# Performance work log

Measured on AMD Instinct MI355X. Metric: run time of the kernel, lower is better.

The kernel has to match this reference:

```python
import jax, jax.numpy as jnp
from jax import lax
import numpy as np

EPSILON = 0.1
GAMMA = 1.0
RHO = 0.5
STOPERR = 1e-6
NUM_ITER_MAX = 1000


def setup_inputs() -> dict:
    key = jax.random.key(0)
    n, k = 131072, 512
    logits = jax.random.normal(key, (n, k), dtype=jnp.float32)
    return {"logits": logits}


def reference(logits):
    # logits is detached in the original (no grad through it)
    logits = lax.stop_gradient(logits)
    # cost = -log softmax over classes
    cost = -jax.nn.log_softmax(logits, axis=1)          # [n, k]
    n, k = cost.shape
    dt = cost.dtype

    # augment with a zero-cost dummy column (the "mu" column)
    expand_cost = jnp.concatenate([cost, jnp.zeros((n, 1), dt)], axis=1)  # [n, k+1]
    Q = jnp.exp(-expand_cost / EPSILON)                  # [n, k+1]

    Pa = jnp.full((n, 1), 1.0 / n, dt)                   # row marginal (equality)
    Pb = jnp.full((k + 1, 1), RHO / k, dt).at[-1].set(1.0 - RHO)  # col marginal
    b0 = jnp.full((k + 1, 1), 1.0 / (k + 1), dt)
    a0 = jnp.zeros((n, 1), dt)
    fi = GAMMA / (GAMMA + EPSILON)

    def cond(state):
        a, b, last_b, err, it = state
        return jnp.logical_and(err > STOPERR, it < NUM_ITER_MAX)

    def body(state):
        a, b, last_b, err, it = state
        a = Pa / (Q @ b)                                 # [n, 1]
        b = Pb / (Q.T @ a)                               # [k+1, 1]
        # semi-relaxed KL step on all but the dummy column
        b = b.at[:-1, :].set(jnp.power(b[:-1, :], fi))
        err = jnp.linalg.norm(b - last_b)
        return (a, b, b, err, it + 1)

    init = (a0, b0, b0, jnp.asarray(1.0, dt), jnp.asarray(0, jnp.int32))
    a, b, _, err, iternum = lax.while_loop(cond, body, init)

    plan = a * Q * b.T                                   # [n, k+1]
    plan = plan * n                                      # final=True scaling
    plan = plan[:, :-1].astype(jnp.float32)              # drop dummy column
    return plan
```

## Files before the change

### kernel.cpp

```cpp
#include <hip/hip_runtime.h>
#include <hip/hip_cooperative_groups.h>

constexpr int   NROWS   = 131072;
constexpr int   KCOLS   = 512;
constexpr int   KP1     = 513;
constexpr float PA      = 1.0f / 131072.0f;
constexpr float PB_REAL = 0.5f / 512.0f;
constexpr float PB_DUM  = 0.5f;
constexpr float FI      = (float)(1.0 / 1.1);
constexpr float STOPERR = 1e-6f;
constexpr int   MAXIT   = 1000;
constexpr float LOG2E   = 1.4426950408889634f;
constexpr float CQ      = 10.0f * LOG2E;
constexpr float LN2     = 0.6931471805599453f;

constexpr int BLOCKS  = 256;
constexpr int THREADS = 1024;
constexpr int WPB     = THREADS / 64;
constexpr int NWAVES  = BLOCKS * WPB;

constexpr size_t OFF_LSE = 0;
constexpr size_t OFF_A   = (size_t)NROWS;
constexpr int    KPAD    = 520;
constexpr size_t OFF_B0  = 2 * (size_t)NROWS;
constexpr size_t OFF_B1  = OFF_B0 + KPAD;
constexpr size_t OFF_BF  = OFF_B0 + 2 * KPAD;
constexpr size_t OFF_EP  = OFF_B0 + 3 * KPAD;
constexpr size_t OFF_CP  = OFF_B0 + 4 * KPAD;
constexpr size_t OFF_BAR = OFF_CP + (size_t)KP1 * BLOCKS;

constexpr size_t QLO_BYTE_OFF = (size_t)NROWS * KCOLS * 2;

__device__ __forceinline__ float waveReduceSum(float v) {
#pragma unroll
  for (int s = 32; s >= 1; s >>= 1) v += __shfl_xor(v, s);
  return v;
}
__device__ __forceinline__ float waveReduceMax(float v) {
#pragma unroll
  for (int s = 32; s >= 1; s >>= 1) v = fmaxf(v, __shfl_xor(v, s));
  return v;
}

__device__ __forceinline__ float scload(const float* p) {
  return __hip_atomic_load(p, __ATOMIC_RELAXED, __HIP_MEMORY_SCOPE_AGENT);
}
__device__ __forceinline__ void scstore(float* p, float v) {
  __hip_atomic_store(p, v, __ATOMIC_RELAXED, __HIP_MEMORY_SCOPE_AGENT);
}

__device__ __forceinline__ void unpack8(const uint4 h, const uint2 l, float q[8]) {
  q[0] = __uint_as_float((h.x << 16)         | ((l.x << 8) & 0xff00u));
  q[1] = __uint_as_float((h.x & 0xffff0000u) | ( l.x       & 0xff00u));
  q[2] = __uint_as_float((h.y << 16)         | ((l.x >> 8) & 0xff00u));
  q[3] = __uint_as_float((h.y & 0xffff0000u) | ((l.x >> 16)& 0xff00u));
  q[4] = __uint_as_float((h.z << 16)         | ((l.y << 8) & 0xff00u));
  q[5] = __uint_as_float((h.z & 0xffff0000u) | ( l.y       & 0xff00u));
  q[6] = __uint_as_float((h.w << 16)         | ((l.y >> 8) & 0xff00u));
  q[7] = __uint_as_float((h.w & 0xffff0000u) | ((l.y >> 16)& 0xff00u));
}

__global__ __launch_bounds__(1024) void lse_q_init_kernel(
    const float* __restrict__ logits, float* __restrict__ ws,
    unsigned short* __restrict__ qhi, unsigned char* __restrict__ qlo) {
  float* lse = ws + OFF_LSE;
  const int nw   = (gridDim.x * blockDim.x) >> 6;
  const int gw   = (blockIdx.x * blockDim.x + threadIdx.x) >> 6;
  const int lane = threadIdx.x & 63;

  for (int r = gw; r < NROWS; r += nw) {
    const float4* row4 = reinterpret_cast<const float4*>(logits + (size_t)r * KCOLS);
    float4 x0 = row4[lane];
    float4 x1 = row4[64 + lane];
    float m = fmaxf(fmaxf(fmaxf(x0.x, x0.y), fmaxf(x0.z, x0.w)),
                    fmaxf(fmaxf(x1.x, x1.y), fmaxf(x1.z, x1.w)));
    m = waveReduceMax(m);
    float s = exp2f((x0.x - m) * LOG2E) + exp2f((x0.y - m) * LOG2E)
            + exp2f((x0.z - m) * LOG2E) + exp2f((x0.w - m) * LOG2E)
            + exp2f((x1.x - m) * LOG2E) + exp2f((x1.y - m) * LOG2E)
            + exp2f((x1.z - m) * LOG2E) + exp2f((x1.w - m) * LOG2E);
    s = waveReduceSum(s);
    float L = m + log2f(s) * LN2;
    if (lane == 0) lse[r] = L;
    unsigned u[8];
    u[0] = __float_as_uint(exp2f((x0.x - L) * CQ)) + 0x80u;
    u[1] = __float_as_uint(exp2f((x0.y - L) * CQ)) + 0x80u;
    u[2] = __float_as_uint(exp2f((x0.z - L) * CQ)) + 0x80u;
    u[3] = __float_as_uint(exp2f((x0.w - L) * CQ)) + 0x80u;
    u[4] = __float_as_uint(exp2f((x1.x - L) * CQ)) + 0x80u;
    u[5] = __float_as_uint(exp2f((x1.y - L) * CQ)) + 0x80u;
    u[6] = __float_as_uint(exp2f((x1.z - L) * CQ)) + 0x80u;
    u[7] = __float_as_uint(exp2f((x1.w - L) * CQ)) + 0x80u;
    ushort4 hA, hB;  uchar4 lA, lB;
    hA.x = (unsigned short)(u[0] >> 16); lA.x = (unsigned char)(u[0] >> 8);
    hA.y = (unsigned short)(u[1] >> 16); lA.y = (unsigned char)(u[1] >> 8);
    hA.z = (unsigned short)(u[2] >> 16); lA.z = (unsigned char)(u[2] >> 8);
    hA.w = (unsigned short)(u[3] >> 16); lA.w = (unsigned char)(u[3] >> 8);
    hB.x = (unsigned short)(u[4] >> 16); lB.x = (unsigned char)(u[4] >> 8);
    hB.y = (unsigned short)(u[5] >> 16); lB.y = (unsigned char)(u[5] >> 8);
    hB.z = (unsigned short)(u[6] >> 16); lB.z = (unsigned char)(u[6] >> 8);
    hB.w = (unsigned short)(u[7] >> 16); lB.w = (unsigned char)(u[7] >> 8);
    *reinterpret_cast<ushort4*>(qhi + (size_t)r * KCOLS + 4 * lane)       = hA;
    *reinterpret_cast<ushort4*>(qhi + (size_t)r * KCOLS + 256 + 4 * lane) = hB;
    *reinterpret_cast<uchar4*>(qlo + (size_t)r * KCOLS + 4 * lane)        = lA;
    *reinterpret_cast<uchar4*>(qlo + (size_t)r * KCOLS + 256 + 4 * lane)  = lB;
  }
  if (blockIdx.x == 0 && threadIdx.x < KP1)
    ws[OFF_B0 + threadIdx.x] = 1.0f / 513.0f;
  if (blockIdx.x == 0 && threadIdx.x == 0) {
    ((unsigned*)(ws + OFF_BAR))[0] = 0u;
    ((unsigned*)(ws + OFF_BAR + 32))[0] = 0u;
  }
}

__global__ __launch_bounds__(THREADS, 4) void sinkhorn_loop(
    const unsigned short* __restrict__ qhi, const unsigned char* __restrict__ qlo,
    float* __restrict__ ws) {
  float* a    = ws + OFF_A;
  float* b0   = ws + OFF_B0;
  float* b1   = ws + OFF_B1;
  float* bfin = ws + OFF_BF;
  float* ep   = ws + OFF_EP;
  float* colp = ws + OFF_CP;
  unsigned* cnt = (unsigned*)(ws + OFF_BAR);
  unsigned* gen = (unsigned*)(ws + OFF_BAR + 32);

  __shared__ float lds[WPB][KPAD];
  __shared__ float s_err;
  __shared__ int   s_nbar;
  __shared__ int   s_dead;

  const int tid  = threadIdx.x;
  const int wv   = tid >> 6;
  const int lane = tid & 63;
  const int bk   = blockIdx.x;
  const int gw   = bk * WPB + wv;

  if (tid == 0) { s_nbar = 0; s_dead = 0; }
  __syncthreads();

  auto gridBar = [&]() {
    __syncthreads();
    if (tid == 0) {
      int nb = s_nbar;
      unsigned old = atomicAdd(cnt, 1u);
      if (old == (unsigned)(nb * BLOCKS + (BLOCKS - 1))) {
        atomicAdd(gen, 1u);
      } else if (!s_dead) {
        int spins = 0;
        while (__hip_atomic_load(gen, __ATOMIC_RELAXED, __HIP_MEMORY_SCOPE_AGENT)
               <= (unsigned)nb) {
          __builtin_amdgcn_s_sleep(1);
          if (++spins > (1 << 24)) { s_dead = 1; break; }
        }
      }
      s_nbar = nb + 1;
    }
    __syncthreads();
  };

  float err = 1.0f;
  int it = 0;
  for (; it < MAXIT; ++it) {
    if (!(err > STOPERR)) break;

    const float* bcv = (it & 1) ? b1 : b0;
    float*       bnv = (it & 1) ? b0 : b1;

    float rb[8];
#pragma unroll
    for (int e = 0; e < 8; ++e) rb[e] = scload(&bcv[8 * lane + e]);
    float bdum = scload(&bcv[512]);

    float cp[8] = {0.f, 0.f, 0.f, 0.f, 0.f, 0.f, 0.f, 0.f};
    float adum = 0.f;
    for (int r = gw; r < NROWS; r += 4 * NWAVES) {
      const int r1 = r + NWAVES, r2 = r + 2 * NWAVES, r3 = r + 3 * NWAVES;
      uint4 h0 = ((const uint4*)(qhi + (size_t)r  * KCOLS))[lane];
      uint4 h1 = ((const uint4*)(qhi + (size_t)r1 * KCOLS))[lane];
      uint4 h2 = ((const uint4*)(qhi + (size_t)r2 * KCOLS))[lane];
      uint4 h3 = ((const uint4*)(qhi + (size_t)r3 * KCOLS))[lane];
      uint2 l0 = ((const uint2*)(qlo + (size_t)r  * KCOLS))[lane];
      uint2 l1 = ((const uint2*)(qlo + (size_t)r1 * KCOLS))[lane];
      uint2 l2 = ((const uint2*)(qlo + (size_t)r2 * KCOLS))[lane];
      uint2 l3 = ((const uint2*)(qlo + (size_t)r3 * KCOLS))[lane];
      float q0[8], q1[8], q2[8], q3[8];
      unpack8(h0, l0, q0);
      unpack8(h1, l1, q1);
      unpack8(h2, l2, q2);
      unpack8(h3, l3, q3);
      float d0 = 0.f, d1 = 0.f, d2 = 0.f, d3 = 0.f;
#pragma unroll
      for (int e = 0; e < 8; ++e) {
        d0 = fmaf(q0[e], rb[e], d0);
        d1 = fmaf(q1[e], rb[e], d1);
        d2 = fmaf(q2[e], rb[e], d2);
        d3 = fmaf(q3[e], rb[e], d3);
      }
#pragma unroll
      for (int s = 32; s >= 1; s >>= 1) {
        d0 += __shfl_xor(d0, s);
        d1 += __shfl_xor(d1, s);
        d2 += __shfl_xor(d2, s);
        d3 += __shfl_xor(d3, s);
      }
      float ai0 = PA / (d0 + bdum);
      float ai1 = PA / (d1 + bdum);
      float ai2 = PA / (d2 + bdum);
      float ai3 = PA / (d3 + bdum);
      if (lane == 0) { a[r] = ai0; a[r1] = ai1; a[r2] = ai2; a[r3] = ai3; }
#pragma unroll
      for (int e = 0; e < 8; ++e) {
        cp[e] = fmaf(ai0, q0[e], cp[e]);
        cp[e] = fmaf(ai1, q1[e], cp[e]);
        cp[e] = fmaf(ai2, q2[e], cp[e]);
        cp[e] = fmaf(ai3, q3[e], cp[e]);
      }
      adum += (ai0 + ai1) + (ai2 + ai3);
    }
#pragma unroll
    for (int e = 0; e < 8; ++e) lds[wv][8 * lane + e] = cp[e];
    if (lane == 0) lds[wv][512] = adum;
    __syncthreads();
    for (int t = tid; t < KP1; t += THREADS) {
      float s = 0.f;
#pragma unroll
      for (int w2 = 0; w2 < WPB; ++w2) s += lds[w2][t];
      scstore(&colp[(size_t)t * BLOCKS + bk], s);
    }
    gridBar();

    {
      int jcol = (wv == 0) ? 2 * bk
               : (wv == 1) ? 2 * bk + 1
               : (bk == 0 && wv == 2) ? 512 : -1;
      if (jcol >= 0) {
        float s = 0.f;
#pragma unroll
        for (int e = 0; e < 4; ++e)
          s += scload(&colp[(size_t)jcol * BLOCKS + 4 * lane + e]);
        s = waveReduceSum(s);
        if (lane == 0) {
          float bj = (jcol < KCOLS) ? powf(PB_REAL / s, FI) : (PB_DUM / s);
          scstore(&bnv[jcol], bj);
          float d = bj - scload(&bcv[jcol]);
          scstore(&ep[jcol], d * d);
        }
      }
    }
    gridBar();

    if (wv == 0) {
      float s = 0.f;
      for (int t = lane; t < KP1; t += 64) s += scload(&ep[t]);
      s = waveReduceSum(s);
      if (lane == 0) s_err = sqrtf(s);
    }
    __syncthreads();
    err = s_err;
  }

  if (bk == 0) {
    const float* bf = (it & 1) ? b1 : b0;
    for (int t = tid; t < KP1; t += THREADS) bfin[t] = scload(&bf[t]);
  }
}

__global__ __launch_bounds__(1024) void plan_epilogue(
    const float* __restrict__ logits, const float* __restrict__ ws,
    float* __restrict__ out) {
  const float* lse  = ws + OFF_LSE;
  const float* a    = ws + OFF_A;
  const float* bfin = ws + OFF_BF;
  const int nw   = (gridDim.x * blockDim.x) >> 6;
  const int gw   = (blockIdx.x * blockDim.x + threadIdx.x) >> 6;
  const int lane = threadIdx.x & 63;

  const float4* b4 = reinterpret_cast<const float4*>(bfin);
  float4 rb0 = b4[lane];
  float4 rb1 = b4[64 + lane];

  for (int r = gw; r < NROWS; r += nw) {
    const float4* row4 = reinterpret_cast<const float4*>(logits + (size_t)r * KCOLS);
    float4*       out4 = reinterpret_cast<float4*>(out + (size_t)r * KCOLS);
    float L  = lse[r];
    float na = a[r] * (float)NROWS;
    float4 x0 = row4[lane];
    float4 x1 = row4[64 + lane];
    float4 o0, o1;
    o0.x = na * exp2f((x0.x - L) * CQ) * rb0.x;
    o0.y = na * exp2f((x0.y - L) * CQ) * rb0.y;
    o0.z = na * exp2f((x0.z - L) * CQ) * rb0.z;
    o0.w = na * exp2f((x0.w - L) * CQ) * rb0.w;
    o1.x = na * exp2f((x1.x - L) * CQ) * rb1.x;
    o1.y = na * exp2f((x1.y - L) * CQ) * rb1.y;
    o1.z = na * exp2f((x1.z - L) * CQ) * rb1.z;
    o1.w = na * exp2f((x1.w - L) * CQ) * rb1.w;
    out4[lane]      = o0;
    out4[64 + lane] = o1;
  }
}

extern "C" void kernel_launch(void* const* d_in, const int* in_sizes, int n_in,
                              void* d_out, int out_size, void* d_ws, size_t ws_size,
                              hipStream_t stream) {
  (void)in_sizes; (void)n_in; (void)out_size; (void)ws_size;
  const float*    logits = (const float*)d_in[0];
  float*          out    = (float*)d_out;
  float*          ws     = (float*)d_ws;
  unsigned short* qhi    = (unsigned short*)d_out;
  unsigned char*  qlo    = (unsigned char*)d_out + QLO_BYTE_OFF;

  hipLaunchKernelGGL(lse_q_init_kernel, dim3(1024), dim3(1024), 0, stream,
                     logits, ws, qhi, qlo);

  const unsigned short* qhArg = qhi;
  const unsigned char*  qlArg = qlo;
  float*                wsArg = ws;
  void* args[] = { (void*)&qhArg, (void*)&qlArg, (void*)&wsArg };
  hipLaunchCooperativeKernel((void*)sinkhorn_loop, dim3(BLOCKS), dim3(THREADS),
                             args, 0, stream);

  hipLaunchKernelGGL(plan_epilogue, dim3(2048), dim3(1024), 0, stream,
                     logits, ws, out);
}
```

Baseline: 18.17 ms.

## Add geometric extrapolation of Sinkhorn b updates and unroll row loop to 8

```diff
diff --git a/kernel.cpp b/kernel.cpp
--- a/kernel.cpp
+++ b/kernel.cpp
@@ -25,11 +25,12 @@
 constexpr size_t OFF_B0  = 2 * (size_t)NROWS;
 constexpr size_t OFF_B1  = OFF_B0 + KPAD;
 constexpr size_t OFF_BF  = OFF_B0 + 2 * KPAD;
-constexpr size_t OFF_EP  = OFF_B0 + 3 * KPAD;
-constexpr size_t OFF_CP  = OFF_B0 + 4 * KPAD;
-constexpr size_t OFF_BAR = OFF_CP + (size_t)KP1 * BLOCKS;
-
-constexpr size_t QLO_BYTE_OFF = (size_t)NROWS * KCOLS * 2;
+constexpr size_t OFF_D0  = OFF_B0 + 3 * KPAD;
+constexpr size_t OFF_D1  = OFF_B0 + 4 * KPAD;
+
+constexpr size_t QLO_BYTE_OFF  = (size_t)NROWS * KCOLS * 2;
+constexpr size_t COLP_BYTE_OFF = 192ull * 1024 * 1024;
+constexpr size_t BAR_BYTE_OFF  = 200ull * 1024 * 1024;
 
 __device__ __forceinline__ float waveReduceSum(float v) {
 #pragma unroll
@@ -62,7 +63,8 @@
 
 __global__ __launch_bounds__(1024) void lse_q_init_kernel(
     const float* __restrict__ logits, float* __restrict__ ws,
-    unsigned short* __restrict__ qhi, unsigned char* __restrict__ qlo) {
+    unsigned short* __restrict__ qhi, unsigned char* __restrict__ qlo,
+    unsigned* __restrict__ bar) {
   float* lse = ws + OFF_LSE;
   const int nw   = (gridDim.x * blockDim.x) >> 6;
   const int gw   = (blockIdx.x * blockDim.x + threadIdx.x) >> 6;
@@ -108,25 +110,25 @@
   if (blockIdx.x == 0 && threadIdx.x < KP1)
     ws[OFF_B0 + threadIdx.x] = 1.0f / 513.0f;
   if (blockIdx.x == 0 && threadIdx.x == 0) {
-    ((unsigned*)(ws + OFF_BAR))[0] = 0u;
-    ((unsigned*)(ws + OFF_BAR + 32))[0] = 0u;
+    bar[0]  = 0u;
+    bar[32] = 0u;
   }
 }
 
 __global__ __launch_bounds__(THREADS, 4) void sinkhorn_loop(
     const unsigned short* __restrict__ qhi, const unsigned char* __restrict__ qlo,
-    float* __restrict__ ws) {
+    float* __restrict__ ws, float* __restrict__ colp, unsigned* __restrict__ bar) {
   float* a    = ws + OFF_A;
   float* b0   = ws + OFF_B0;
   float* b1   = ws + OFF_B1;
   float* bfin = ws + OFF_BF;
-  float* ep   = ws + OFF_EP;
-  float* colp = ws + OFF_CP;
-  unsigned* cnt = (unsigned*)(ws + OFF_BAR);
-  unsigned* gen = (unsigned*)(ws + OFF_BAR + 32);
+  float* dl0  = ws + OFF_D0;
+  float* dl1  = ws + OFF_D1;
+  unsigned* cnt = bar;
+  unsigned* gen = bar + 32;
 
   __shared__ float lds[WPB][KPAD];
-  __shared__ float s_err;
+  __shared__ float s_err, s_s1, s_s2;
   __shared__ int   s_nbar;
   __shared__ int   s_dead;
 
@@ -166,6 +168,8 @@
 
     const float* bcv = (it & 1) ? b1 : b0;
     float*       bnv = (it & 1) ? b0 : b1;
+    float*       dcu = (it & 1) ? dl1 : dl0;
+    const float* dpr = (it & 1) ? dl0 : dl1;
 
     float rb[8];
 #pragma unroll
@@ -174,49 +178,44 @@
 
     float cp[8] = {0.f, 0.f, 0.f, 0.f, 0.f, 0.f, 0.f, 0.f};
     float adum = 0.f;
-    for (int r = gw; r < NROWS; r += 4 * NWAVES) {
-      const int r1 = r + NWAVES, r2 = r + 2 * NWAVES, r3 = r + 3 * NWAVES;
-      uint4 h0 = ((const uint4*)(qhi + (size_t)r  * KCOLS))[lane];
-      uint4 h1 = ((const uint4*)(qhi + (size_t)r1 * KCOLS))[lane];
-      uint4 h2 = ((const uint4*)(qhi + (size_t)r2 * KCOLS))[lane];
-      uint4 h3 = ((const uint4*)(qhi + (size_t)r3 * KCOLS))[lane];
-      uint2 l0 = ((const uint2*)(qlo + (size_t)r  * KCOLS))[lane];
-      uint2 l1 = ((const uint2*)(qlo + (size_t)r1 * KCOLS))[lane];
-      uint2 l2 = ((const uint2*)(qlo + (size_t)r2 * KCOLS))[lane];
-      uint2 l3 = ((const uint2*)(qlo + (size_t)r3 * KCOLS))[lane];
-      float q0[8], q1[8], q2[8], q3[8];
-      unpack8(h0, l0, q0);
-      unpack8(h1, l1, q1);
-      unpack8(h2, l2, q2);
-      unpack8(h3, l3, q3);
-      float d0 = 0.f, d1 = 0.f, d2 = 0.f, d3 = 0.f;
-#pragma unroll
-      for (int e = 0; e < 8; ++e) {
-        d0 = fmaf(q0[e], rb[e], d0);
-        d1 = fmaf(q1[e], rb[e], d1);
-        d2 = fmaf(q2[e], rb[e], d2);
-        d3 = fmaf(q3[e], rb[e], d3);
+    for (int r = gw; r < NROWS; r += 8 * NWAVES) {
+      uint4 h[8];  uint2 l[8];
+#pragma unroll
+      for (int u = 0; u < 8; ++u) {
+        const int rr = r + u * NWAVES;
+        h[u] = ((const uint4*)(qhi + (size_t)rr * KCOLS))[lane];
+        l[u] = ((const uint2*)(qlo + (size_t)rr * KCOLS))[lane];
+      }
+      float d[8];
+#pragma unroll
+      for (int u = 0; u < 8; ++u) {
+        float q[8];
+        unpack8(h[u], l[u], q);
+        float dd = 0.f;
+#pragma unroll
+        for (int e = 0; e < 8; ++e) dd = fmaf(q[e], rb[e], dd);
+        d[u] = dd;
       }
 #pragma unroll
       for (int s = 32; s >= 1; s >>= 1) {
-        d0 += __shfl_xor(d0, s);
-        d1 += __shfl_xor(d1, s);
-        d2 += __shfl_xor(d2, s);
-        d3 += __shfl_xor(d3, s);
-      }
-      float ai0 = PA / (d0 + bdum);
-      float ai1 = PA / (d1 + bdum);
-      float ai2 = PA / (d2 + bdum);
-      float ai3 = PA / (d3 + bdum);
-      if (lane == 0) { a[r] = ai0; a[r1] = ai1; a[r2] = ai2; a[r3] = ai3; }
-#pragma unroll
-      for (int e = 0; e < 8; ++e) {
-        cp[e] = fmaf(ai0, q0[e], cp[e]);
-        cp[e] = fmaf(ai1, q1[e], cp[e]);
-        cp[e] = fmaf(ai2, q2[e], cp[e]);
-        cp[e] = fmaf(ai3, q3[e], cp[e]);
-      }
-      adum += (ai0 + ai1) + (ai2 + ai3);
+#pragma unroll
+        for (int u = 0; u < 8; ++u) d[u] += __shfl_xor(d[u], s);
+      }
+      float ai[8];
+#pragma unroll
+      for (int u = 0; u < 8; ++u) ai[u] = PA / (d[u] + bdum);
+      if (lane == 0) {
+#pragma unroll
+        for (int u = 0; u < 8; ++u) a[r + u * NWAVES] = ai[u];
+      }
+#pragma unroll
+      for (int u = 0; u < 8; ++u) {
+        float q[8];
+        unpack8(h[u], l[u], q);
+#pragma unroll
+        for (int e = 0; e < 8; ++e) cp[e] = fmaf(ai[u], q[e], cp[e]);
+        adum += ai[u];
+      }
     }
 #pragma unroll
     for (int e = 0; e < 8; ++e) lds[wv][8 * lane + e] = cp[e];
@@ -243,21 +242,44 @@
         if (lane == 0) {
           float bj = (jcol < KCOLS) ? powf(PB_REAL / s, FI) : (PB_DUM / s);
           scstore(&bnv[jcol], bj);
-          float d = bj - scload(&bcv[jcol]);
-          scstore(&ep[jcol], d * d);
+          scstore(&dcu[jcol], bj - scload(&bcv[jcol]));
         }
       }
     }
     gridBar();
 
     if (wv == 0) {
-      float s = 0.f;
-      for (int t = lane; t < KP1; t += 64) s += scload(&ep[t]);
-      s = waveReduceSum(s);
-      if (lane == 0) s_err = sqrtf(s);
+      float s0 = 0.f, s1 = 0.f, s2 = 0.f;
+      for (int t = lane; t < KP1; t += 64) {
+        float dc = scload(&dcu[t]);
+        float dp = scload(&dpr[t]);
+        s0 += dc * dc;  s1 += dc * dp;  s2 += dp * dp;
+      }
+#pragma unroll
+      for (int s = 32; s >= 1; s >>= 1) {
+        s0 += __shfl_xor(s0, s);
+        s1 += __shfl_xor(s1, s);
+        s2 += __shfl_xor(s2, s);
+      }
+      if (lane == 0) { s_err = sqrtf(s0); s_s1 = s1; s_s2 = s2; }
     }
     __syncthreads();
     err = s_err;
+
+    if ((it & 7) == 7 && err > 10.0f * STOPERR) {
+      float rho = (s_s2 > 0.f) ? (s_s1 / s_s2) : 0.f;
+      if (rho > 0.5f && rho < 0.95f) {
+        float c = rho / (1.0f - rho);
+        int jcol = (wv == 0) ? 2 * bk
+                 : (wv == 1) ? 2 * bk + 1
+                 : (bk == 0 && wv == 2) ? 512 : -1;
+        if (jcol >= 0 && lane == 0) {
+          float bx = scload(&bnv[jcol]) + c * scload(&dcu[jcol]);
+          if (bx > 1e-30f) scstore(&bnv[jcol], bx);
+        }
+        gridBar();
+      }
+    }
   }
 
   if (bk == 0) {
@@ -310,14 +332,19 @@
   float*          ws     = (float*)d_ws;
   unsigned short* qhi    = (unsigned short*)d_out;
   unsigned char*  qlo    = (unsigned char*)d_out + QLO_BYTE_OFF;
+  float*          colp   = (float*)((char*)d_out + COLP_BYTE_OFF);
+  unsigned*       bar    = (unsigned*)((char*)d_out + BAR_BYTE_OFF);
 
   hipLaunchKernelGGL(lse_q_init_kernel, dim3(1024), dim3(1024), 0, stream,
-                     logits, ws, qhi, qlo);
+                     logits, ws, qhi, qlo, bar);
 
   const unsigned short* qhArg = qhi;
   const unsigned char*  qlArg = qlo;
   float*                wsArg = ws;
-  void* args[] = { (void*)&qhArg, (void*)&qlArg, (void*)&wsArg };
+  float*                cpArg = colp;
+  unsigned*             brArg = bar;
+  void* args[] = { (void*)&qhArg, (void*)&qlArg, (void*)&wsArg,
+                   (void*)&cpArg, (void*)&brArg };
   hipLaunchCooperativeKernel((void*)sinkhorn_loop, dim3(BLOCKS), dim3(THREADS),
                              args, 0, stream);
 
```

After: 22.81 ms. 25.5% more time.

## Add Aitken-style b extrapolation and scale Sinkhorn loop to 512 blocks

Applied to the files above, without the earlier changes.

```diff
diff --git a/kernel.cpp b/kernel.cpp
--- a/kernel.cpp
+++ b/kernel.cpp
@@ -14,22 +14,21 @@
 constexpr float CQ      = 10.0f * LOG2E;
 constexpr float LN2     = 0.6931471805599453f;
 
-constexpr int BLOCKS  = 256;
 constexpr int THREADS = 1024;
 constexpr int WPB     = THREADS / 64;
-constexpr int NWAVES  = BLOCKS * WPB;
 
 constexpr size_t OFF_LSE = 0;
 constexpr size_t OFF_A   = (size_t)NROWS;
-constexpr int    KPAD    = 520;
+constexpr int    KPAD    = 516;
 constexpr size_t OFF_B0  = 2 * (size_t)NROWS;
 constexpr size_t OFF_B1  = OFF_B0 + KPAD;
 constexpr size_t OFF_BF  = OFF_B0 + 2 * KPAD;
-constexpr size_t OFF_EP  = OFF_B0 + 3 * KPAD;
-constexpr size_t OFF_CP  = OFF_B0 + 4 * KPAD;
-constexpr size_t OFF_BAR = OFF_CP + (size_t)KP1 * BLOCKS;
-
-constexpr size_t QLO_BYTE_OFF = (size_t)NROWS * KCOLS * 2;
+constexpr size_t OFF_D0  = OFF_B0 + 3 * KPAD;
+constexpr size_t OFF_D1  = OFF_B0 + 4 * KPAD;
+
+constexpr size_t QLO_BYTE_OFF  = (size_t)NROWS * KCOLS * 2;
+constexpr size_t COLP_BYTE_OFF = 192ull * 1024 * 1024;
+constexpr size_t BAR_BYTE_OFF  = 200ull * 1024 * 1024;
 
 __device__ __forceinline__ float waveReduceSum(float v) {
 #pragma unroll
@@ -62,7 +61,8 @@
 
 __global__ __launch_bounds__(1024) void lse_q_init_kernel(
     const float* __restrict__ logits, float* __restrict__ ws,
-    unsigned short* __restrict__ qhi, unsigned char* __restrict__ qlo) {
+    unsigned short* __restrict__ qhi, unsigned char* __restrict__ qlo,
+    unsigned* __restrict__ bar) {
   float* lse = ws + OFF_LSE;
   const int nw   = (gridDim.x * blockDim.x) >> 6;
   const int gw   = (blockIdx.x * blockDim.x + threadIdx.x) >> 6;
@@ -108,24 +108,25 @@
   if (blockIdx.x == 0 && threadIdx.x < KP1)
     ws[OFF_B0 + threadIdx.x] = 1.0f / 513.0f;
   if (blockIdx.x == 0 && threadIdx.x == 0) {
-    ((unsigned*)(ws + OFF_BAR))[0] = 0u;
-    ((unsigned*)(ws + OFF_BAR + 32))[0] = 0u;
-  }
-}
-
-__global__ __launch_bounds__(THREADS, 4) void sinkhorn_loop(
+    bar[0]  = 0u;
+    bar[32] = 0u;
+  }
+}
+
+template <int NBLK>
+__global__ __launch_bounds__(THREADS, 8) void sinkhorn_loop(
     const unsigned short* __restrict__ qhi, const unsigned char* __restrict__ qlo,
-    float* __restrict__ ws) {
+    float* __restrict__ ws, float* __restrict__ colp, unsigned* __restrict__ bar) {
   float* a    = ws + OFF_A;
   float* b0   = ws + OFF_B0;
   float* b1   = ws + OFF_B1;
   float* bfin = ws + OFF_BF;
-  float* ep   = ws + OFF_EP;
-  float* colp = ws + OFF_CP;
-  unsigned* cnt = (unsigned*)(ws + OFF_BAR);
-  unsigned* gen = (unsigned*)(ws + OFF_BAR + 32);
-
-  __shared__ float lds[WPB][KPAD];
+  float* dl0  = ws + OFF_D0;
+  float* dl1  = ws + OFF_D1;
+  unsigned* cnt = bar;
+  unsigned* gen = bar + 32;
+
+  __shared__ float lds[8][KPAD];
   __shared__ float s_err;
   __shared__ int   s_nbar;
   __shared__ int   s_dead;
@@ -135,6 +136,7 @@
   const int lane = tid & 63;
   const int bk   = blockIdx.x;
   const int gw   = bk * WPB + wv;
+  const int NWV  = NBLK * WPB;
 
   if (tid == 0) { s_nbar = 0; s_dead = 0; }
   __syncthreads();
@@ -144,7 +146,7 @@
     if (tid == 0) {
       int nb = s_nbar;
       unsigned old = atomicAdd(cnt, 1u);
-      if (old == (unsigned)(nb * BLOCKS + (BLOCKS - 1))) {
+      if (old == (unsigned)(nb * NBLK + (NBLK - 1))) {
         atomicAdd(gen, 1u);
       } else if (!s_dead) {
         int spins = 0;
@@ -166,6 +168,8 @@
 
     const float* bcv = (it & 1) ? b1 : b0;
     float*       bnv = (it & 1) ? b0 : b1;
+    float*       dcu = (it & 1) ? dl1 : dl0;
+    const float* dpr = (it & 1) ? dl0 : dl1;
 
     float rb[8];
 #pragma unroll
@@ -174,8 +178,8 @@
 
     float cp[8] = {0.f, 0.f, 0.f, 0.f, 0.f, 0.f, 0.f, 0.f};
     float adum = 0.f;
-    for (int r = gw; r < NROWS; r += 4 * NWAVES) {
-      const int r1 = r + NWAVES, r2 = r + 2 * NWAVES, r3 = r + 3 * NWAVES;
+    for (int r = gw; r < NROWS; r += 4 * NWV) {
+      const int r1 = r + NWV, r2 = r + 2 * NWV, r3 = r + 3 * NWV;
       uint4 h0 = ((const uint4*)(qhi + (size_t)r  * KCOLS))[lane];
       uint4 h1 = ((const uint4*)(qhi + (size_t)r1 * KCOLS))[lane];
       uint4 h2 = ((const uint4*)(qhi + (size_t)r2 * KCOLS))[lane];
@@ -218,46 +222,76 @@
       }
       adum += (ai0 + ai1) + (ai2 + ai3);
     }
-#pragma unroll
-    for (int e = 0; e < 8; ++e) lds[wv][8 * lane + e] = cp[e];
-    if (lane == 0) lds[wv][512] = adum;
+    if (wv >= 8) {
+#pragma unroll
+      for (int e = 0; e < 8; ++e) lds[wv - 8][8 * lane + e] = cp[e];
+      if (lane == 0) lds[wv - 8][512] = adum;
+    }
+    __syncthreads();
+    if (wv < 8) {
+#pragma unroll
+      for (int e = 0; e < 8; ++e) cp[e] += lds[wv][8 * lane + e];
+      if (lane == 0) adum += lds[wv][512];
+    }
+    __syncthreads();
+    if (wv < 8) {
+#pragma unroll
+      for (int e = 0; e < 8; ++e) lds[wv][8 * lane + e] = cp[e];
+      if (lane == 0) lds[wv][512] = adum;
+    }
     __syncthreads();
     for (int t = tid; t < KP1; t += THREADS) {
       float s = 0.f;
 #pragma unroll
-      for (int w2 = 0; w2 < WPB; ++w2) s += lds[w2][t];
-      scstore(&colp[(size_t)t * BLOCKS + bk], s);
+      for (int w2 = 0; w2 < 8; ++w2) s += lds[w2][t];
+      scstore(&colp[(size_t)t * NBLK + bk], s);
     }
     gridBar();
 
     {
-      int jcol = (wv == 0) ? 2 * bk
-               : (wv == 1) ? 2 * bk + 1
-               : (bk == 0 && wv == 2) ? 512 : -1;
-      if (jcol >= 0) {
+      const int jcol = bk + wv * NBLK;
+      if (jcol < KP1) {
         float s = 0.f;
 #pragma unroll
-        for (int e = 0; e < 4; ++e)
-          s += scload(&colp[(size_t)jcol * BLOCKS + 4 * lane + e]);
+        for (int e = 0; e < NBLK / 64; ++e)
+          s += scload(&colp[(size_t)jcol * NBLK + 64 * e + lane]);
         s = waveReduceSum(s);
         if (lane == 0) {
           float bj = (jcol < KCOLS) ? powf(PB_REAL / s, FI) : (PB_DUM / s);
           scstore(&bnv[jcol], bj);
-          float d = bj - scload(&bcv[jcol]);
-          scstore(&ep[jcol], d * d);
+          scstore(&dcu[jcol], bj - scload(&bcv[jcol]));
         }
       }
     }
     gridBar();
 
     if (wv == 0) {
-      float s = 0.f;
-      for (int t = lane; t < KP1; t += 64) s += scload(&ep[t]);
-      s = waveReduceSum(s);
-      if (lane == 0) s_err = sqrtf(s);
+      float s0 = 0.f;
+      for (int t = lane; t < KP1; t += 64) {
+        float dc = scload(&dcu[t]);
+        s0 += dc * dc;
+      }
+      s0 = waveReduceSum(s0);
+      if (lane == 0) s_err = sqrtf(s0);
     }
     __syncthreads();
     err = s_err;
+
+    if ((it & 7) == 7 && it >= 15 && err > 100.0f * STOPERR) {
+      const int jcol = bk + wv * NBLK;
+      if (jcol < KP1 && lane == 0) {
+        float dc = scload(&dcu[jcol]);
+        float dp = scload(&dpr[jcol]);
+        if (fabsf(dp) > 1e-37f) {
+          float rr = dc / dp;
+          if (rr > -0.97f && rr < 0.95f) {
+            float bx = scload(&bnv[jcol]) + (rr / (1.0f - rr)) * dc;
+            if (bx > 1e-30f) scstore(&bnv[jcol], bx);
+          }
+        }
+      }
+      gridBar();
+    }
   }
 
   if (bk == 0) {
@@ -310,16 +344,34 @@
   float*          ws     = (float*)d_ws;
   unsigned short* qhi    = (unsigned short*)d_out;
   unsigned char*  qlo    = (unsigned char*)d_out + QLO_BYTE_OFF;
+  float*          colp   = (float*)((char*)d_out + COLP_BYTE_OFF);
+  unsigned*       bar    = (unsigned*)((char*)d_out + BAR_BYTE_OFF);
 
   hipLaunchKernelGGL(lse_q_init_kernel, dim3(1024), dim3(1024), 0, stream,
-                     logits, ws, qhi, qlo);
+                     logits, ws, qhi, qlo, bar);
 
   const unsigned short* qhArg = qhi;
   const unsigned char*  qlArg = qlo;
   float*                wsArg = ws;
-  void* args[] = { (void*)&qhArg, (void*)&qlArg, (void*)&wsArg };
-  hipLaunchCooperativeKernel((void*)sinkhorn_loop, dim3(BLOCKS), dim3(THREADS),
-                             args, 0, stream);
+  float*                cpArg = colp;
+  unsigned*             brArg = bar;
+  void* args[] = { (void*)&qhArg, (void*)&qlArg, (void*)&wsArg,
+                   (void*)&cpArg, (void*)&brArg };
+
+  void (*k512)(const unsigned short*, const unsigned char*, float*, float*,
+               unsigned*) = sinkhorn_loop<512>;
+  void (*k256)(const unsigned short*, const unsigned char*, float*, float*,
+               unsigned*) = sinkhorn_loop<256>;
+  int nbPerCU = 0;
+  (void)hipOccupancyMaxActiveBlocksPerMultiprocessor(&nbPerCU, (const void*)k512,
+                                                     THREADS, 0);
+  if (nbPerCU >= 2) {
+    hipLaunchCooperativeKernel((void*)k512, dim3(512), dim3(THREADS),
+                               args, 0, stream);
+  } else {
+    hipLaunchCooperativeKernel((void*)k256, dim3(256), dim3(THREADS),
+                               args, 0, stream);
+  }
 
   hipLaunchKernelGGL(plan_epilogue, dim3(2048), dim3(1024), 0, stream,
                      logits, ws, out);
```

Measured after the change: 38.58 ms. +112.3%, slower.

## Pack Q as contiguous 24-bit rows per wave and stream via async global-to-LDS ring

Applied to the files above, without the earlier changes.

```diff
diff --git a/kernel.cpp b/kernel.cpp
--- a/kernel.cpp
+++ b/kernel.cpp
@@ -1,5 +1,4 @@
 #include <hip/hip_runtime.h>
-#include <hip/hip_cooperative_groups.h>
 
 constexpr int   NROWS   = 131072;
 constexpr int   KCOLS   = 512;
@@ -16,8 +15,17 @@
 
 constexpr int BLOCKS  = 256;
 constexpr int THREADS = 1024;
-constexpr int WPB     = THREADS / 64;
-constexpr int NWAVES  = BLOCKS * WPB;
+constexpr int WPB     = 16;
+constexpr int NWV     = BLOCKS * WPB;
+constexpr int RPW     = NROWS / NWV;
+constexpr int NP      = RPW / 2;
+
+constexpr int DP     = 3;
+constexpr int ROWB   = 1536;
+constexpr int PAIRB  = 2 * ROWB;
+constexpr int RING_B = DP * PAIRB;
+constexpr size_t LDS_RING  = (size_t)WPB * RING_B;
+constexpr size_t LDS_TOTAL = LDS_RING + WPB * RPW * 4;
 
 constexpr size_t OFF_LSE = 0;
 constexpr size_t OFF_A   = (size_t)NROWS;
@@ -26,10 +34,20 @@
 constexpr size_t OFF_B1  = OFF_B0 + KPAD;
 constexpr size_t OFF_BF  = OFF_B0 + 2 * KPAD;
 constexpr size_t OFF_EP  = OFF_B0 + 3 * KPAD;
-constexpr size_t OFF_CP  = OFF_B0 + 4 * KPAD;
-constexpr size_t OFF_BAR = OFF_CP + (size_t)KP1 * BLOCKS;
-
-constexpr size_t QLO_BYTE_OFF = (size_t)NROWS * KCOLS * 2;
+
+constexpr size_t COLP_BYTE_OFF = 192ull * 1024 * 1024;
+constexpr size_t BAR_BYTE_OFF  = 200ull * 1024 * 1024;
+
+#define WAITVM(N) do { asm volatile("s_waitcnt vmcnt(" #N ")" ::: "memory"); \
+                       __builtin_amdgcn_sched_barrier(0); } while (0)
+#define WAITLG() do { asm volatile("s_waitcnt lgkmcnt(0)" ::: "memory"); \
+                      __builtin_amdgcn_sched_barrier(0); } while (0)
+
+__device__ __forceinline__ void glds16(const void* g, void* l) {
+  __builtin_amdgcn_global_load_lds(
+      (const __attribute__((address_space(1))) void*)g,
+      (__attribute__((address_space(3))) void*)l, 16, 0, 0);
+}
 
 __device__ __forceinline__ float waveReduceSum(float v) {
 #pragma unroll
@@ -49,20 +67,22 @@
   __hip_atomic_store(p, v, __ATOMIC_RELAXED, __HIP_MEMORY_SCOPE_AGENT);
 }
 
-__device__ __forceinline__ void unpack8(const uint4 h, const uint2 l, float q[8]) {
-  q[0] = __uint_as_float((h.x << 16)         | ((l.x << 8) & 0xff00u));
-  q[1] = __uint_as_float((h.x & 0xffff0000u) | ( l.x       & 0xff00u));
-  q[2] = __uint_as_float((h.y << 16)         | ((l.x >> 8) & 0xff00u));
-  q[3] = __uint_as_float((h.y & 0xffff0000u) | ((l.x >> 16)& 0xff00u));
-  q[4] = __uint_as_float((h.z << 16)         | ((l.y << 8) & 0xff00u));
-  q[5] = __uint_as_float((h.z & 0xffff0000u) | ( l.y       & 0xff00u));
-  q[6] = __uint_as_float((h.w << 16)         | ((l.y >> 8) & 0xff00u));
-  q[7] = __uint_as_float((h.w & 0xffff0000u) | ((l.y >> 16)& 0xff00u));
+__device__ __forceinline__ void pack_chunk(const unsigned u[4], unsigned w[3]) {
+  w[0] = u[0] | (u[1] << 24);
+  w[1] = (u[1] >> 8) | (u[2] << 16);
+  w[2] = (u[2] >> 16) | (u[3] << 8);
+}
+__device__ __forceinline__ void unpack_chunk(const unsigned* p, float q[4]) {
+  unsigned a0 = p[0], a1 = p[1], a2 = p[2];
+  q[0] = __uint_as_float(a0 << 8);
+  q[1] = __uint_as_float(((a0 >> 16) & 0x0000FF00u) | (a1 << 16));
+  q[2] = __uint_as_float(((a1 >> 8) & 0x00FFFF00u) | (a2 << 24));
+  q[3] = __uint_as_float(a2 & 0xFFFFFF00u);
 }
 
 __global__ __launch_bounds__(1024) void lse_q_init_kernel(
     const float* __restrict__ logits, float* __restrict__ ws,
-    unsigned short* __restrict__ qhi, unsigned char* __restrict__ qlo) {
+    unsigned char* __restrict__ q24, unsigned* __restrict__ bar) {
   float* lse = ws + OFF_LSE;
   const int nw   = (gridDim.x * blockDim.x) >> 6;
   const int gw   = (blockIdx.x * blockDim.x + threadIdx.x) >> 6;
@@ -82,50 +102,45 @@
     s = waveReduceSum(s);
     float L = m + log2f(s) * LN2;
     if (lane == 0) lse[r] = L;
-    unsigned u[8];
-    u[0] = __float_as_uint(exp2f((x0.x - L) * CQ)) + 0x80u;
-    u[1] = __float_as_uint(exp2f((x0.y - L) * CQ)) + 0x80u;
-    u[2] = __float_as_uint(exp2f((x0.z - L) * CQ)) + 0x80u;
-    u[3] = __float_as_uint(exp2f((x0.w - L) * CQ)) + 0x80u;
-    u[4] = __float_as_uint(exp2f((x1.x - L) * CQ)) + 0x80u;
-    u[5] = __float_as_uint(exp2f((x1.y - L) * CQ)) + 0x80u;
-    u[6] = __float_as_uint(exp2f((x1.z - L) * CQ)) + 0x80u;
-    u[7] = __float_as_uint(exp2f((x1.w - L) * CQ)) + 0x80u;
-    ushort4 hA, hB;  uchar4 lA, lB;
-    hA.x = (unsigned short)(u[0] >> 16); lA.x = (unsigned char)(u[0] >> 8);
-    hA.y = (unsigned short)(u[1] >> 16); lA.y = (unsigned char)(u[1] >> 8);
-    hA.z = (unsigned short)(u[2] >> 16); lA.z = (unsigned char)(u[2] >> 8);
-    hA.w = (unsigned short)(u[3] >> 16); lA.w = (unsigned char)(u[3] >> 8);
-    hB.x = (unsigned short)(u[4] >> 16); lB.x = (unsigned char)(u[4] >> 8);
-    hB.y = (unsigned short)(u[5] >> 16); lB.y = (unsigned char)(u[5] >> 8);
-    hB.z = (unsigned short)(u[6] >> 16); lB.z = (unsigned char)(u[6] >> 8);
-    hB.w = (unsigned short)(u[7] >> 16); lB.w = (unsigned char)(u[7] >> 8);
-    *reinterpret_cast<ushort4*>(qhi + (size_t)r * KCOLS + 4 * lane)       = hA;
-    *reinterpret_cast<ushort4*>(qhi + (size_t)r * KCOLS + 256 + 4 * lane) = hB;
-    *reinterpret_cast<uchar4*>(qlo + (size_t)r * KCOLS + 4 * lane)        = lA;
-    *reinterpret_cast<uchar4*>(qlo + (size_t)r * KCOLS + 256 + 4 * lane)  = lB;
+    unsigned uA[4], uB[4];
+    uA[0] = (__float_as_uint(exp2f((x0.x - L) * CQ)) + 0x80u) >> 8;
+    uA[1] = (__float_as_uint(exp2f((x0.y - L) * CQ)) + 0x80u) >> 8;
+    uA[2] = (__float_as_uint(exp2f((x0.z - L) * CQ)) + 0x80u) >> 8;
+    uA[3] = (__float_as_uint(exp2f((x0.w - L) * CQ)) + 0x80u) >> 8;
+    uB[0] = (__float_as_uint(exp2f((x1.x - L) * CQ)) + 0x80u) >> 8;
+    uB[1] = (__float_as_uint(exp2f((x1.y - L) * CQ)) + 0x80u) >> 8;
+    uB[2] = (__float_as_uint(exp2f((x1.z - L) * CQ)) + 0x80u) >> 8;
+    uB[3] = (__float_as_uint(exp2f((x1.w - L) * CQ)) + 0x80u) >> 8;
+    unsigned wA[3], wB[3];
+    pack_chunk(uA, wA);
+    pack_chunk(uB, wB);
+    size_t ro = ((size_t)(r & (NWV - 1)) * RPW + (size_t)(r >> 12)) * ROWB;
+    unsigned* pA = (unsigned*)(q24 + ro + 12 * lane);
+    unsigned* pB = (unsigned*)(q24 + ro + 768 + 12 * lane);
+    pA[0] = wA[0]; pA[1] = wA[1]; pA[2] = wA[2];
+    pB[0] = wB[0]; pB[1] = wB[1]; pB[2] = wB[2];
   }
   if (blockIdx.x == 0 && threadIdx.x < KP1)
     ws[OFF_B0 + threadIdx.x] = 1.0f / 513.0f;
   if (blockIdx.x == 0 && threadIdx.x == 0) {
-    ((unsigned*)(ws + OFF_BAR))[0] = 0u;
-    ((unsigned*)(ws + OFF_BAR + 32))[0] = 0u;
-  }
-}
-
-__global__ __launch_bounds__(THREADS, 4) void sinkhorn_loop(
-    const unsigned short* __restrict__ qhi, const unsigned char* __restrict__ qlo,
-    float* __restrict__ ws) {
+    bar[0]  = 0u;
+    bar[32] = 0u;
+  }
+}
+
+extern __shared__ char smem[];
+
+__global__ __launch_bounds__(THREADS) void sinkhorn_loop(
+    const unsigned char* __restrict__ q24, float* __restrict__ ws,
+    float* __restrict__ colp, unsigned* __restrict__ bar) {
   float* a    = ws + OFF_A;
   float* b0   = ws + OFF_B0;
   float* b1   = ws + OFF_B1;
   float* bfin = ws + OFF_BF;
   float* ep   = ws + OFF_EP;
-  float* colp = ws + OFF_CP;
-  unsigned* cnt = (unsigned*)(ws + OFF_BAR);
-  unsigned* gen = (unsigned*)(ws + OFF_BAR + 32);
-
-  __shared__ float lds[WPB][KPAD];
+  unsigned* cnt = bar;
+  unsigned* gen = bar + 32;
+
   __shared__ float s_err;
   __shared__ int   s_nbar;
   __shared__ int   s_dead;
@@ -135,6 +150,12 @@
   const int lane = tid & 63;
   const int bk   = blockIdx.x;
   const int gw   = bk * WPB + wv;
+
+  char*  ring  = smem + wv * RING_B;
+  float* a_lds = (float*)(smem + LDS_RING) + wv * RPW;
+  float (*lds2)[KPAD] = (float(*)[KPAD])smem;
+
+  const char* gwave = (const char*)q24 + (size_t)gw * RPW * ROWB;
 
   if (tid == 0) { s_nbar = 0; s_dead = 0; }
   __syncthreads();
@@ -172,73 +193,87 @@
     for (int e = 0; e < 8; ++e) rb[e] = scload(&bcv[8 * lane + e]);
     float bdum = scload(&bcv[512]);
 
+#pragma unroll
+    for (int s = 0; s < DP; ++s) {
+      const char* g = gwave + (size_t)s * PAIRB;
+      char* lsl = ring + s * PAIRB;
+      glds16(g + 16 * lane,        lsl);
+      glds16(g + 1024 + 16 * lane, lsl + 1024);
+      glds16(g + 2048 + 16 * lane, lsl + 2048);
+    }
+
     float cp[8] = {0.f, 0.f, 0.f, 0.f, 0.f, 0.f, 0.f, 0.f};
     float adum = 0.f;
-    for (int r = gw; r < NROWS; r += 4 * NWAVES) {
-      const int r1 = r + NWAVES, r2 = r + 2 * NWAVES, r3 = r + 3 * NWAVES;
-      uint4 h0 = ((const uint4*)(qhi + (size_t)r  * KCOLS))[lane];
-      uint4 h1 = ((const uint4*)(qhi + (size_t)r1 * KCOLS))[lane];
-      uint4 h2 = ((const uint4*)(qhi + (size_t)r2 * KCOLS))[lane];
-      uint4 h3 = ((const uint4*)(qhi + (size_t)r3 * KCOLS))[lane];
-      uint2 l0 = ((const uint2*)(qlo + (size_t)r  * KCOLS))[lane];
-      uint2 l1 = ((const uint2*)(qlo + (size_t)r1 * KCOLS))[lane];
-      uint2 l2 = ((const uint2*)(qlo + (size_t)r2 * KCOLS))[lane];
-      uint2 l3 = ((const uint2*)(qlo + (size_t)r3 * KCOLS))[lane];
-      float q0[8], q1[8], q2[8], q3[8];
-      unpack8(h0, l0, q0);
-      unpack8(h1, l1, q1);
-      unpack8(h2, l2, q2);
-      unpack8(h3, l3, q3);
-      float d0 = 0.f, d1 = 0.f, d2 = 0.f, d3 = 0.f;
+    int so = 0;
+#pragma unroll 1
+    for (int p = 0; p < NP; ++p) {
+      if (p <= NP - 3)      WAITVM(6);
+      else if (p == NP - 2) WAITVM(3);
+      else                  WAITVM(0);
+
+      const char* sl = ring + so * PAIRB;
+      const unsigned* p0 = (const unsigned*)(sl + 24 * lane);
+      const unsigned* p1 = (const unsigned*)(sl + ROWB + 24 * lane);
+      float q0[8], q1[8];
+      unpack_chunk(p0,     q0);
+      unpack_chunk(p0 + 3, q0 + 4);
+      unpack_chunk(p1,     q1);
+      unpack_chunk(p1 + 3, q1 + 4);
+      WAITLG();
+
+      if (p + DP < NP) {
+        const char* g = gwave + (size_t)(p + DP) * PAIRB;
+        char* lsl = ring + so * PAIRB;
+        glds16(g + 16 * lane,        lsl);
+        glds16(g + 1024 + 16 * lane, lsl + 1024);
+        glds16(g + 2048 + 16 * lane, lsl + 2048);
+      }
+
+      float d0 = 0.f, d1 = 0.f;
 #pragma unroll
       for (int e = 0; e < 8; ++e) {
         d0 = fmaf(q0[e], rb[e], d0);
         d1 = fmaf(q1[e], rb[e], d1);
-        d2 = fmaf(q2[e], rb[e], d2);
-        d3 = fmaf(q3[e], rb[e], d3);
       }
 #pragma unroll
       for (int s = 32; s >= 1; s >>= 1) {
         d0 += __shfl_xor(d0, s);
         d1 += __shfl_xor(d1, s);
-        d2 += __shfl_xor(d2, s);
-        d3 += __shfl_xor(d3, s);
       }
       float ai0 = PA / (d0 + bdum);
       float ai1 = PA / (d1 + bdum);
-      float ai2 = PA / (d2 + bdum);
-      float ai3 = PA / (d3 + bdum);
-      if (lane == 0) { a[r] = ai0; a[r1] = ai1; a[r2] = ai2; a[r3] = ai3; }
+      if (lane == 0) { a_lds[2 * p] = ai0; a_lds[2 * p + 1] = ai1; }
 #pragma unroll
       for (int e = 0; e < 8; ++e) {
         cp[e] = fmaf(ai0, q0[e], cp[e]);
         cp[e] = fmaf(ai1, q1[e], cp[e]);
-        cp[e] = fmaf(ai2, q2[e], cp[e]);
-        cp[e] = fmaf(ai3, q3[e], cp[e]);
-      }
-      adum += (ai0 + ai1) + (ai2 + ai3);
-    }
-#pragma unroll
-    for (int e = 0; e < 8; ++e) lds[wv][8 * lane + e] = cp[e];
-    if (lane == 0) lds[wv][512] = adum;
+      }
+      adum += ai0 + ai1;
+      so = (so == DP - 1) ? 0 : so + 1;
+    }
+
+    if (lane < RPW) a[gw + lane * NWV] = a_lds[lane];
+    __syncthreads();
+
+#pragma unroll
+    for (int e = 0; e < 8; ++e) lds2[wv][8 * lane + e] = cp[e];
+    if (lane == 0) lds2[wv][512] = adum;
     __syncthreads();
     for (int t = tid; t < KP1; t += THREADS) {
       float s = 0.f;
 #pragma unroll
-      for (int w2 = 0; w2 < WPB; ++w2) s += lds[w2][t];
+      for (int w2 = 0; w2 < WPB; ++w2) s += lds2[w2][t];
       scstore(&colp[(size_t)t * BLOCKS + bk], s);
     }
     gridBar();
 
     {
-      int jcol = (wv == 0) ? 2 * bk
-               : (wv == 1) ? 2 * bk + 1
-               : (bk == 0 && wv == 2) ? 512 : -1;
-      if (jcol >= 0) {
+      const int jcol = bk + wv * BLOCKS;
+      if (jcol < KP1) {
         float s = 0.f;
 #pragma unroll
-        for (int e = 0; e < 4; ++e)
-          s += scload(&colp[(size_t)jcol * BLOCKS + 4 * lane + e]);
+        for (int e = 0; e < BLOCKS / 64; ++e)
+          s += scload(&colp[(size_t)jcol * BLOCKS + 64 * e + lane]);
         s = waveReduceSum(s);
         if (lane == 0) {
           float bj = (jcol < KCOLS) ? powf(PB_REAL / s, FI) : (PB_DUM / s);
@@ -251,10 +286,10 @@
     gridBar();
 
     if (wv == 0) {
-      float s = 0.f;
-      for (int t = lane; t < KP1; t += 64) s += scload(&ep[t]);
-      s = waveReduceSum(s);
-      if (lane == 0) s_err = sqrtf(s);
+      float s0 = 0.f;
+      for (int t = lane; t < KP1; t += 64) s0 += scload(&ep[t]);
+      s0 = waveReduceSum(s0);
+      if (lane == 0) s_err = sqrtf(s0);
     }
     __syncthreads();
     err = s_err;
@@ -305,21 +340,26 @@
                               void* d_out, int out_size, void* d_ws, size_t ws_size,
                               hipStream_t stream) {
   (void)in_sizes; (void)n_in; (void)out_size; (void)ws_size;
-  const float*    logits = (const float*)d_in[0];
-  float*          out    = (float*)d_out;
-  float*          ws     = (float*)d_ws;
-  unsigned short* qhi    = (unsigned short*)d_out;
-  unsigned char*  qlo    = (unsigned char*)d_out + QLO_BYTE_OFF;
+  const float*   logits = (const float*)d_in[0];
+  float*         out    = (float*)d_out;
+  float*         ws     = (float*)d_ws;
+  unsigned char* q24    = (unsigned char*)d_out;
+  float*         colp   = (float*)((char*)d_out + COLP_BYTE_OFF);
+  unsigned*      bar    = (unsigned*)((char*)d_out + BAR_BYTE_OFF);
 
   hipLaunchKernelGGL(lse_q_init_kernel, dim3(1024), dim3(1024), 0, stream,
-                     logits, ws, qhi, qlo);
-
-  const unsigned short* qhArg = qhi;
-  const unsigned char*  qlArg = qlo;
-  float*                wsArg = ws;
-  void* args[] = { (void*)&qhArg, (void*)&qlArg, (void*)&wsArg };
+                     logits, ws, q24, bar);
+
+  (void)hipFuncSetAttribute((const void*)sinkhorn_loop,
+                            hipFuncAttributeMaxDynamicSharedMemorySize,
+                            (int)LDS_TOTAL);
+  const unsigned char* qArg  = q24;
+  float*               wsArg = ws;
+  float*               cpArg = colp;
+  unsigned*            brArg = bar;
+  void* args[] = { (void*)&qArg, (void*)&wsArg, (void*)&cpArg, (void*)&brArg };
   hipLaunchCooperativeKernel((void*)sinkhorn_loop, dim3(BLOCKS), dim3(THREADS),
-                             args, 0, stream);
+                             args, (unsigned)LDS_TOTAL, stream);
 
   hipLaunchKernelGGL(plan_epilogue, dim3(2048), dim3(1024), 0, stream,
                      logits, ws, out);
```

Result: faster. 17.78 ms (-2.1%).
